# Optimization experiments

Measured on AMD Instinct MI355X. Metric: run time of the kernel, lower is better.

The kernel has to match this reference:

```python
import jax, jax.numpy as jnp
import numpy as np

GAMMA = 0.01
EPS = 0.01

def setup_inputs() -> dict:
    key = jax.random.key(0)
    k1, k2, k3 = jax.random.split(key, 3)
    B, T, IND, WIDTH = 512, 512, 64, 128
    x = jax.random.normal(k1, (B, T, IND), dtype=jnp.float32)
    init_state = jnp.zeros((1, B, WIDTH), dtype=jnp.float32)
    # xavier-uniform-like init for W and V
    lim_w = float(np.sqrt(6.0 / (WIDTH + WIDTH)))
    lim_v = float(np.sqrt(6.0 / (IND + WIDTH)))
    W = jax.random.uniform(k2, (WIDTH, WIDTH), jnp.float32, -lim_w, lim_w)
    V = jax.random.uniform(k3, (IND, WIDTH), jnp.float32, -lim_v, lim_v)
    b = jnp.zeros((WIDTH,), dtype=jnp.float32)
    return {"x": x, "init_state": init_state, "W": W, "V": V, "b": b}

def reference(x, init_state, W, V, b):
    # x: [B, T, ind]; init_state: [1, B, width]
    A = W - W.T  # antisymmetric matrix, computed once
    xV = jnp.einsum('bti,iw->btw', x, V) + b  # precompute input projection

    def step(state, u):
        # state: [B, width]; u: [B, width] (projected input at timestep t)
        new_state = state + EPS * jnp.tanh(state @ A - GAMMA * state + u)
        return new_state, new_state

    state0 = init_state[0]
    final_state, outputs = jax.lax.scan(step, state0, jnp.swapaxes(xV, 0, 1))
    outputs = jnp.swapaxes(outputs, 0, 1)  # [B, T, width]
    return outputs, final_state
```

## Files before the change

kernel.cpp:

```cpp
#include <hip/hip_runtime.h>
#include <hip/hip_bf16.h>

#define B_DIM 512
#define T_DIM 512
#define IND 64
#define WIDTH 128
#define GAMMA 0.01f
#define EPS 0.01f

#define PJ_ROWS 16
#define PJ_NT ((B_DIM * T_DIM) / PJ_ROWS)

__global__ __launch_bounds__(256) void proj_kernel(
    const float* __restrict__ x, const float* __restrict__ V,
    const float* __restrict__ bias, float* __restrict__ out) {
  __shared__ __align__(16) float xs[PJ_ROWS * IND];

  const int tid = threadIdx.x;
  const int c2 = (tid & 63) * 2;
  const int rh = tid >> 6;

  float2 Vreg[IND];
#pragma unroll
  for (int k = 0; k < IND; ++k)
    Vreg[k] = *(const float2*)(V + k * WIDTH + c2);
  const float2 bb = *(const float2*)(bias + c2);

  for (int tile = blockIdx.x; tile < PJ_NT; tile += gridDim.x) {
    const size_t m0 = (size_t)tile * PJ_ROWS;
    __syncthreads();
#pragma unroll
    for (int q = 0; q < 4; ++q)
      xs[tid + 256 * q] = x[m0 * IND + tid + 256 * q];
    __syncthreads();

    float2 acc0 = bb, acc1 = bb, acc2 = bb, acc3 = bb;
#pragma unroll
    for (int k4 = 0; k4 < IND / 4; ++k4) {
      float4 xv0 = ((const float4*)&xs[(rh + 0) * IND])[k4];
      float4 xv1 = ((const float4*)&xs[(rh + 4) * IND])[k4];
      float4 xv2 = ((const float4*)&xs[(rh + 8) * IND])[k4];
      float4 xv3 = ((const float4*)&xs[(rh + 12) * IND])[k4];
#pragma unroll
      for (int j = 0; j < 4; ++j) {
        float2 v = Vreg[4 * k4 + j];
        float e0 = (j == 0) ? xv0.x : (j == 1) ? xv0.y : (j == 2) ? xv0.z : xv0.w;
        float e1 = (j == 0) ? xv1.x : (j == 1) ? xv1.y : (j == 2) ? xv1.z : xv1.w;
        float e2 = (j == 0) ? xv2.x : (j == 1) ? xv2.y : (j == 2) ? xv2.z : xv2.w;
        float e3 = (j == 0) ? xv3.x : (j == 1) ? xv3.y : (j == 2) ? xv3.z : xv3.w;
        acc0.x += e0 * v.x; acc0.y += e0 * v.y;
        acc1.x += e1 * v.x; acc1.y += e1 * v.y;
        acc2.x += e2 * v.x; acc2.y += e2 * v.y;
        acc3.x += e3 * v.x; acc3.y += e3 * v.y;
      }
    }
    *(float2*)(out + (m0 + rh + 0) * WIDTH + c2) = acc0;
    *(float2*)(out + (m0 + rh + 4) * WIDTH + c2) = acc1;
    *(float2*)(out + (m0 + rh + 8) * WIDTH + c2) = acc2;
    *(float2*)(out + (m0 + rh + 12) * WIDTH + c2) = acc3;
  }
}

template <int CTRL>
__device__ __forceinline__ float dpp_mov(float x) {
  return __int_as_float(
      __builtin_amdgcn_update_dpp(0, __float_as_int(x), CTRL, 0xf, 0xf, true));
}

__global__ __launch_bounds__(256) void rnn_kernel(
    const float* __restrict__ W, const float* __restrict__ init,
    float* __restrict__ out, float* __restrict__ finals) {
  __shared__ __align__(16) float sL[2][WIDTH];
  const int b = blockIdx.x;
  const int tid = threadIdx.x;
  const int kc = tid & 3;
  const int cp = tid >> 2;
  const int c0 = 2 * cp;

  float Areg[2][32];
  {
    const int k0 = kc * 32;
#pragma unroll
    for (int j = 0; j < 8; ++j) {
      const int ri = (j + 2 * kc) & 7;
      const int k = k0 + ri * 4;
#pragma unroll
      for (int col = 0; col < 2; ++col) {
        const int cc = c0 + col;
        float4 wr = *(const float4*)(W + (size_t)cc * WIDTH + k);
        Areg[col][4 * j + 0] = W[(size_t)(k + 0) * WIDTH + cc] - wr.x;
        Areg[col][4 * j + 1] = W[(size_t)(k + 1) * WIDTH + cc] - wr.y;
        Areg[col][4 * j + 2] = W[(size_t)(k + 2) * WIDTH + cc] - wr.z;
        Areg[col][4 * j + 3] = W[(size_t)(k + 3) * WIDTH + cc] - wr.w;
      }
    }
  }

  float2 s = *(const float2*)(init + (size_t)b * WIDTH + c0);
  if (kc == 0) *(float2*)&sL[0][c0] = s;
  __syncthreads();

  const float* uc = out + (size_t)b * T_DIM * WIDTH + c0;
  float* outc = out + (size_t)b * T_DIM * WIDTH + c0;
  float2 u0 = *(const float2*)(uc);
  float2 u1 = *(const float2*)(uc + WIDTH);

#pragma unroll 1
  for (int t = 0; t < T_DIM; ++t) {
    const int p = t & 1;
    const float2 u = u0;
    u0 = u1;
    if (t + 2 < T_DIM) u1 = *(const float2*)(uc + (size_t)(t + 2) * WIDTH);

    const float4* sp = (const float4*)&sL[p][0];
    float a00 = 0.f, a01 = 0.f, a10 = 0.f, a11 = 0.f;
#pragma unroll
    for (int j = 0; j < 8; ++j) {
      const int ri = (j + 2 * kc) & 7;
      float4 sv = sp[kc * 8 + ri];
      a00 += sv.x * Areg[0][4 * j + 0];
      a01 += sv.y * Areg[0][4 * j + 1];
      a00 += sv.z * Areg[0][4 * j + 2];
      a01 += sv.w * Areg[0][4 * j + 3];
      a10 += sv.x * Areg[1][4 * j + 0];
      a11 += sv.y * Areg[1][4 * j + 1];
      a10 += sv.z * Areg[1][4 * j + 2];
      a11 += sv.w * Areg[1][4 * j + 3];
    }
    float d0 = a00 + a01;
    float d1 = a10 + a11;
    d0 += dpp_mov<0xB1>(d0);
    d1 += dpp_mov<0xB1>(d1);
    d0 += dpp_mov<0x4E>(d0);
    d1 += dpp_mov<0x4E>(d1);

    const float f0 = d0 - GAMMA * s.x + u.x;
    const float f1 = d1 - GAMMA * s.y + u.y;
    const float e0 = __expf(2.0f * f0);
    const float e1 = __expf(2.0f * f1);
    const float th0 = fmaf(-2.0f, __builtin_amdgcn_rcpf(e0 + 1.0f), 1.0f);
    const float th1 = fmaf(-2.0f, __builtin_amdgcn_rcpf(e1 + 1.0f), 1.0f);
    s.x = fmaf(EPS, th0, s.x);
    s.y = fmaf(EPS, th1, s.y);

    if (kc == 0) {
      *(float2*)(outc + (size_t)t * WIDTH) = s;
      *(float2*)&sL[p ^ 1][c0] = s;
    }
    __syncthreads();
  }

  if (kc == 0) *(float2*)(finals + (size_t)b * WIDTH + c0) = s;
}

extern "C" void kernel_launch(void* const* d_in, const int* in_sizes, int n_in,
                              void* d_out, int out_size, void* d_ws,
                              size_t ws_size, hipStream_t stream) {
  const float* x = (const float*)d_in[0];
  const float* init = (const float*)d_in[1];
  const float* W = (const float*)d_in[2];
  const float* V = (const float*)d_in[3];
  const float* bias = (const float*)d_in[4];

  float* out = (float*)d_out;
  float* finals = out + (size_t)B_DIM * T_DIM * WIDTH;

  proj_kernel<<<2048, 256, 0, stream>>>(x, V, bias, out);
  rnn_kernel<<<B_DIM, 256, 0, stream>>>(W, init, out, finals);
}
```

Measured before the change: 301.8 us.

## Halve RNN block size so each thread computes four output columns

The recurrent kernel now runs 128 threads per batch row instead of 256, and each thread owns four state columns with a 4x32 register slice of the antisymmetric matrix. This doubles per-thread work and register use while halving the number of waves taking part in each per-timestep barrier and LDS exchange. It also widens the state and input loads and stores to float4. The cost is higher register pressure (128 floats for A alone) and a longer serial dependency chain per step.

```diff
diff --git a/kernel.cpp b/kernel.cpp
--- a/kernel.cpp
+++ b/kernel.cpp
@@ -67,17 +67,17 @@
       __builtin_amdgcn_update_dpp(0, __float_as_int(x), CTRL, 0xf, 0xf, true));
 }
 
-__global__ __launch_bounds__(256) void rnn_kernel(
+__global__ __launch_bounds__(128) void rnn_kernel(
     const float* __restrict__ W, const float* __restrict__ init,
     float* __restrict__ out, float* __restrict__ finals) {
   __shared__ __align__(16) float sL[2][WIDTH];
   const int b = blockIdx.x;
   const int tid = threadIdx.x;
   const int kc = tid & 3;
-  const int cp = tid >> 2;
-  const int c0 = 2 * cp;
+  const int c4 = tid >> 2;
+  const int c0 = 4 * c4;
 
-  float Areg[2][32];
+  float Areg[4][32];
   {
     const int k0 = kc * 32;
 #pragma unroll
@@ -85,7 +85,7 @@
       const int ri = (j + 2 * kc) & 7;
       const int k = k0 + ri * 4;
 #pragma unroll
-      for (int col = 0; col < 2; ++col) {
+      for (int col = 0; col < 4; ++col) {
         const int cc = c0 + col;
         float4 wr = *(const float4*)(W + (size_t)cc * WIDTH + k);
         Areg[col][4 * j + 0] = W[(size_t)(k + 0) * WIDTH + cc] - wr.x;
@@ -96,61 +96,63 @@
     }
   }
 
-  float2 s = *(const float2*)(init + (size_t)b * WIDTH + c0);
-  if (kc == 0) *(float2*)&sL[0][c0] = s;
+  float4 s = *(const float4*)(init + (size_t)b * WIDTH + c0);
+  if (kc == 0) *(float4*)&sL[0][c0] = s;
   __syncthreads();
 
-  const float* uc = out + (size_t)b * T_DIM * WIDTH + c0;
   float* outc = out + (size_t)b * T_DIM * WIDTH + c0;
-  float2 u0 = *(const float2*)(uc);
-  float2 u1 = *(const float2*)(uc + WIDTH);
+  float4 u0 = *(const float4*)(outc);
+  float4 u1 = *(const float4*)(outc + WIDTH);
 
 #pragma unroll 1
   for (int t = 0; t < T_DIM; ++t) {
     const int p = t & 1;
-    const float2 u = u0;
+    const float4 u = u0;
     u0 = u1;
-    if (t + 2 < T_DIM) u1 = *(const float2*)(uc + (size_t)(t + 2) * WIDTH);
+    if (t + 2 < T_DIM) u1 = *(const float4*)(outc + (size_t)(t + 2) * WIDTH);
 
     const float4* sp = (const float4*)&sL[p][0];
-    float a00 = 0.f, a01 = 0.f, a10 = 0.f, a11 = 0.f;
+    float a0[4], a1[4];
+#pragma unroll
+    for (int col = 0; col < 4; ++col) { a0[col] = 0.f; a1[col] = 0.f; }
 #pragma unroll
     for (int j = 0; j < 8; ++j) {
       const int ri = (j + 2 * kc) & 7;
       float4 sv = sp[kc * 8 + ri];
-      a00 += sv.x * Areg[0][4 * j + 0];
-      a01 += sv.y * Areg[0][4 * j + 1];
-      a00 += sv.z * Areg[0][4 * j + 2];
-      a01 += sv.w * Areg[0][4 * j + 3];
-      a10 += sv.x * Areg[1][4 * j + 0];
-      a11 += sv.y * Areg[1][4 * j + 1];
-      a10 += sv.z * Areg[1][4 * j + 2];
-      a11 += sv.w * Areg[1][4 * j + 3];
+#pragma unroll
+      for (int col = 0; col < 4; ++col) {
+        a0[col] += sv.x * Areg[col][4 * j + 0];
+        a1[col] += sv.y * Areg[col][4 * j + 1];
+        a0[col] += sv.z * Areg[col][4 * j + 2];
+        a1[col] += sv.w * Areg[col][4 * j + 3];
+      }
     }
-    float d0 = a00 + a01;
-    float d1 = a10 + a11;
-    d0 += dpp_mov<0xB1>(d0);
-    d1 += dpp_mov<0xB1>(d1);
-    d0 += dpp_mov<0x4E>(d0);
-    d1 += dpp_mov<0x4E>(d1);
+    float d[4];
+#pragma unroll
+    for (int col = 0; col < 4; ++col) d[col] = a0[col] + a1[col];
+#pragma unroll
+    for (int col = 0; col < 4; ++col) d[col] += dpp_mov<0xB1>(d[col]);
+#pragma unroll
+    for (int col = 0; col < 4; ++col) d[col] += dpp_mov<0x4E>(d[col]);
 
-    const float f0 = d0 - GAMMA * s.x + u.x;
-    const float f1 = d1 - GAMMA * s.y + u.y;
-    const float e0 = __expf(2.0f * f0);
-    const float e1 = __expf(2.0f * f1);
-    const float th0 = fmaf(-2.0f, __builtin_amdgcn_rcpf(e0 + 1.0f), 1.0f);
-    const float th1 = fmaf(-2.0f, __builtin_amdgcn_rcpf(e1 + 1.0f), 1.0f);
-    s.x = fmaf(EPS, th0, s.x);
-    s.y = fmaf(EPS, th1, s.y);
+    float* sa = (float*)&s;
+    const float* ua = (const float*)&u;
+#pragma unroll
+    for (int col = 0; col < 4; ++col) {
+      const float f = d[col] - GAMMA * sa[col] + ua[col];
+      const float e = __expf(2.0f * f);
+      const float th = fmaf(-2.0f, __builtin_amdgcn_rcpf(e + 1.0f), 1.0f);
+      sa[col] = fmaf(EPS, th, sa[col]);
+    }
 
     if (kc == 0) {
-      *(float2*)(outc + (size_t)t * WIDTH) = s;
-      *(float2*)&sL[p ^ 1][c0] = s;
+      *(float4*)(outc + (size_t)t * WIDTH) = s;
+      *(float4*)&sL[p ^ 1][c0] = s;
     }
     __syncthreads();
   }
 
-  if (kc == 0) *(float2*)(finals + (size_t)b * WIDTH + c0) = s;
+  if (kc == 0) *(float4*)(finals + (size_t)b * WIDTH + c0) = s;
 }
 
 extern "C" void kernel_launch(void* const* d_in, const int* in_sizes, int n_in,
@@ -166,5 +168,5 @@
   float* finals = out + (size_t)B_DIM * T_DIM * WIDTH;
 
   proj_kernel<<<2048, 256, 0, stream>>>(x, V, bias, out);
-  rnn_kernel<<<B_DIM, 256, 0, stream>>>(W, init, out, finals);
+  rnn_kernel<<<B_DIM, 128, 0, stream>>>(W, init, out, finals);
 }
```

Measured after the change: 341.8 us. +13.2%, slower.

## Process two batch rows per RNN block to reuse register-held A matrix

Applied to the files above, without the earlier changes.

Each RNN block now advances two independent batch rows through the recurrence instead of one. The antisymmetric matrix in registers is shared across both rows, and the per-step barrier, reduction and tanh latency are amortised over twice the work. The grid halves to 256 blocks, which may underfill the GPU's CUs and lengthen each block's serial step time.

```diff
diff --git a/kernel.cpp b/kernel.cpp
--- a/kernel.cpp
+++ b/kernel.cpp
@@ -70,8 +70,9 @@
 __global__ __launch_bounds__(256) void rnn_kernel(
     const float* __restrict__ W, const float* __restrict__ init,
     float* __restrict__ out, float* __restrict__ finals) {
-  __shared__ __align__(16) float sL[2][WIDTH];
-  const int b = blockIdx.x;
+  __shared__ __align__(16) float sL[2][2][WIDTH];
+  const int rA = blockIdx.x * 2;
+  const int rB = rA + 1;
   const int tid = threadIdx.x;
   const int kc = tid & 3;
   const int cp = tid >> 2;
@@ -96,61 +97,95 @@
     }
   }
 
-  float2 s = *(const float2*)(init + (size_t)b * WIDTH + c0);
-  if (kc == 0) *(float2*)&sL[0][c0] = s;
+  float2 sA = *(const float2*)(init + (size_t)rA * WIDTH + c0);
+  float2 sB = *(const float2*)(init + (size_t)rB * WIDTH + c0);
+  if (kc == 0) {
+    *(float2*)&sL[0][0][c0] = sA;
+    *(float2*)&sL[0][1][c0] = sB;
+  }
   __syncthreads();
 
-  const float* uc = out + (size_t)b * T_DIM * WIDTH + c0;
-  float* outc = out + (size_t)b * T_DIM * WIDTH + c0;
-  float2 u0 = *(const float2*)(uc);
-  float2 u1 = *(const float2*)(uc + WIDTH);
+  float* outA = out + (size_t)rA * T_DIM * WIDTH + c0;
+  float* outB = out + (size_t)rB * T_DIM * WIDTH + c0;
+  float2 uA0 = *(const float2*)(outA);
+  float2 uA1 = *(const float2*)(outA + WIDTH);
+  float2 uB0 = *(const float2*)(outB);
+  float2 uB1 = *(const float2*)(outB + WIDTH);
 
 #pragma unroll 1
   for (int t = 0; t < T_DIM; ++t) {
     const int p = t & 1;
-    const float2 u = u0;
-    u0 = u1;
-    if (t + 2 < T_DIM) u1 = *(const float2*)(uc + (size_t)(t + 2) * WIDTH);
-
-    const float4* sp = (const float4*)&sL[p][0];
-    float a00 = 0.f, a01 = 0.f, a10 = 0.f, a11 = 0.f;
+    const float2 uA = uA0, uB = uB0;
+    uA0 = uA1;
+    uB0 = uB1;
+    if (t + 2 < T_DIM) {
+      uA1 = *(const float2*)(outA + (size_t)(t + 2) * WIDTH);
+      uB1 = *(const float2*)(outB + (size_t)(t + 2) * WIDTH);
+    }
+
+    const float4* spA = (const float4*)&sL[p][0][0];
+    const float4* spB = (const float4*)&sL[p][1][0];
+    float aA00 = 0.f, aA01 = 0.f, aA10 = 0.f, aA11 = 0.f;
+    float aB00 = 0.f, aB01 = 0.f, aB10 = 0.f, aB11 = 0.f;
 #pragma unroll
     for (int j = 0; j < 8; ++j) {
       const int ri = (j + 2 * kc) & 7;
-      float4 sv = sp[kc * 8 + ri];
-      a00 += sv.x * Areg[0][4 * j + 0];
-      a01 += sv.y * Areg[0][4 * j + 1];
-      a00 += sv.z * Areg[0][4 * j + 2];
-      a01 += sv.w * Areg[0][4 * j + 3];
-      a10 += sv.x * Areg[1][4 * j + 0];
-      a11 += sv.y * Areg[1][4 * j + 1];
-      a10 += sv.z * Areg[1][4 * j + 2];
-      a11 += sv.w * Areg[1][4 * j + 3];
-    }
-    float d0 = a00 + a01;
-    float d1 = a10 + a11;
-    d0 += dpp_mov<0xB1>(d0);
-    d1 += dpp_mov<0xB1>(d1);
-    d0 += dpp_mov<0x4E>(d0);
-    d1 += dpp_mov<0x4E>(d1);
-
-    const float f0 = d0 - GAMMA * s.x + u.x;
-    const float f1 = d1 - GAMMA * s.y + u.y;
-    const float e0 = __expf(2.0f * f0);
-    const float e1 = __expf(2.0f * f1);
-    const float th0 = fmaf(-2.0f, __builtin_amdgcn_rcpf(e0 + 1.0f), 1.0f);
-    const float th1 = fmaf(-2.0f, __builtin_amdgcn_rcpf(e1 + 1.0f), 1.0f);
-    s.x = fmaf(EPS, th0, s.x);
-    s.y = fmaf(EPS, th1, s.y);
+      float4 vA = spA[kc * 8 + ri];
+      float4 vB = spB[kc * 8 + ri];
+      aA00 += vA.x * Areg[0][4 * j + 0];
+      aA01 += vA.y * Areg[0][4 * j + 1];
+      aA00 += vA.z * Areg[0][4 * j + 2];
+      aA01 += vA.w * Areg[0][4 * j + 3];
+      aA10 += vA.x * Areg[1][4 * j + 0];
+      aA11 += vA.y * Areg[1][4 * j + 1];
+      aA10 += vA.z * Areg[1][4 * j + 2];
+      aA11 += vA.w * Areg[1][4 * j + 3];
+      aB00 += vB.x * Areg[0][4 * j + 0];
+      aB01 += vB.y * Areg[0][4 * j + 1];
+      aB00 += vB.z * Areg[0][4 * j + 2];
+      aB01 += vB.w * Areg[0][4 * j + 3];
+      aB10 += vB.x * Areg[1][4 * j + 0];
+      aB11 += vB.y * Areg[1][4 * j + 1];
+      aB10 += vB.z * Areg[1][4 * j + 2];
+      aB11 += vB.w * Areg[1][4 * j + 3];
+    }
+    float dA0 = aA00 + aA01, dA1 = aA10 + aA11;
+    float dB0 = aB00 + aB01, dB1 = aB10 + aB11;
+    dA0 += dpp_mov<0xB1>(dA0);
+    dA1 += dpp_mov<0xB1>(dA1);
+    dB0 += dpp_mov<0xB1>(dB0);
+    dB1 += dpp_mov<0xB1>(dB1);
+    dA0 += dpp_mov<0x4E>(dA0);
+    dA1 += dpp_mov<0x4E>(dA1);
+    dB0 += dpp_mov<0x4E>(dB0);
+    dB1 += dpp_mov<0x4E>(dB1);
+
+    const float fA0 = dA0 - GAMMA * sA.x + uA.x;
+    const float fA1 = dA1 - GAMMA * sA.y + uA.y;
+    const float fB0 = dB0 - GAMMA * sB.x + uB.x;
+    const float fB1 = dB1 - GAMMA * sB.y + uB.y;
+    const float eA0 = __expf(2.0f * fA0);
+    const float eA1 = __expf(2.0f * fA1);
+    const float eB0 = __expf(2.0f * fB0);
+    const float eB1 = __expf(2.0f * fB1);
+    sA.x = fmaf(EPS, fmaf(-2.0f, __builtin_amdgcn_rcpf(eA0 + 1.0f), 1.0f), sA.x);
+    sA.y = fmaf(EPS, fmaf(-2.0f, __builtin_amdgcn_rcpf(eA1 + 1.0f), 1.0f), sA.y);
+    sB.x = fmaf(EPS, fmaf(-2.0f, __builtin_amdgcn_rcpf(eB0 + 1.0f), 1.0f), sB.x);
+    sB.y = fmaf(EPS, fmaf(-2.0f, __builtin_amdgcn_rcpf(eB1 + 1.0f), 1.0f), sB.y);
 
     if (kc == 0) {
-      *(float2*)(outc + (size_t)t * WIDTH) = s;
-      *(float2*)&sL[p ^ 1][c0] = s;
+      *(float2*)(outA + (size_t)t * WIDTH) = sA;
+      *(float2*)(outB + (size_t)t * WIDTH) = sB;
+      *(float2*)&sL[p ^ 1][0][c0] = sA;
+      *(float2*)&sL[p ^ 1][1][c0] = sB;
     }
     __syncthreads();
   }
 
-  if (kc == 0) *(float2*)(finals + (size_t)b * WIDTH + c0) = s;
+  if (kc == 0) {
+    *(float2*)(finals + (size_t)rA * WIDTH + c0) = sA;
+    *(float2*)(finals + (size_t)rB * WIDTH + c0) = sB;
+  }
 }
 
 extern "C" void kernel_launch(void* const* d_in, const int* in_sizes, int n_in,
@@ -166,5 +201,5 @@
   float* finals = out + (size_t)B_DIM * T_DIM * WIDTH;
 
   proj_kernel<<<2048, 256, 0, stream>>>(x, V, bias, out);
-  rnn_kernel<<<B_DIM, 256, 0, stream>>>(W, init, out, finals);
-}
+  rnn_kernel<<<B_DIM / 2, 256, 0, stream>>>(W, init, out, finals);
+}
```

Measured after the change: 338.1 us. +12.0%, slower.
